# Performance work log

Hardware: AMD Instinct MI355X
Metric: run time of the kernel (lower is better)

The kernel has to match this reference:

```python
import jax, jax.numpy as jnp
import numpy as np

N = 100000      # nodes
E = 1600000     # directed edges (avg degree 16)
DIN, DH, DOUT = 128, 128, 64


def gcn_conv(x, W, b, src, dst, n):
    """PyG GCNConv: out = D^{-1/2} (A + I) D^{-1/2} (x @ W) + b.
    src/dst already include self-loops."""
    deg = jax.ops.segment_sum(jnp.ones_like(src, dtype=x.dtype), dst, num_segments=n)
    dinv = jnp.where(deg > 0, jax.lax.rsqrt(deg), jnp.zeros_like(deg))
    norm = dinv[src] * dinv[dst]                      # [E+N]
    h = x @ W                                         # [N, dout] linear first (PyG)
    msg = h[src] * norm[:, None]                      # gather + scale, [E+N, dout]
    return jax.ops.segment_sum(msg, dst, num_segments=n) + b


def setup_inputs() -> dict:
    key = jax.random.key(0)
    k1, k2, k3 = jax.random.split(key, 3)
    x = jax.random.normal(k1, (N, DIN), dtype=jnp.float32)
    edge_index = jax.random.randint(k2, (2, E), 0, N, dtype=jnp.int64)
    kw1, kw2 = jax.random.split(k3)
    # glorot-style init for the two GCN linear weights
    W1 = jax.random.normal(kw1, (DIN, DH), dtype=jnp.float32) * (1.0 / np.sqrt(DIN))
    b1 = jnp.zeros((DH,), dtype=jnp.float32)
    W2 = jax.random.normal(kw2, (DH, DOUT), dtype=jnp.float32) * (1.0 / np.sqrt(DH))
    b2 = jnp.zeros((DOUT,), dtype=jnp.float32)
    return {"x": x, "W1": W1, "b1": b1, "W2": W2, "b2": b2, "edge_index": edge_index}


def reference(x, W1, b1, W2, b2, edge_index):
    n = x.shape[0]
    loops = jnp.arange(n, dtype=edge_index.dtype)
    src = jnp.concatenate([edge_index[0], loops])     # add self-loops
    dst = jnp.concatenate([edge_index[1], loops])
    h = jax.nn.relu(gcn_conv(x, W1, b1, src, dst, n))
    return gcn_conv(h, W2, b2, src, dst, n)
```

## Files before the change

kernel.cpp:

```cpp
#include <hip/hip_runtime.h>

#define N_NODES 100000
#define N_EDGES 1600000
#define BUCKET_SHIFT 9
#define NB 196
#define BIN_BLOCKS 782
#define GEMM_BLOCKS 1563
#define BCAP 10240

typedef short bf16x8 __attribute__((ext_vector_type(8)));
typedef float f32x4 __attribute__((ext_vector_type(4)));

__device__ __forceinline__ unsigned short f2bf(float f) {
    unsigned int u = __float_as_uint(f);
    unsigned int r = (u + 0x7FFFu + ((u >> 16) & 1u)) >> 16;
    return (unsigned short)r;
}
__device__ __forceinline__ float bf2f(unsigned short b) {
    return __uint_as_float(((unsigned int)b) << 16);
}

__global__ __launch_bounds__(256) void k_tw(const float* __restrict__ W1, const float* __restrict__ W2,
                                            unsigned short* __restrict__ w1t, unsigned short* __restrict__ w2t,
                                            int* __restrict__ bcur) {
    int t = blockIdx.x * 256 + threadIdx.x;
    if (t < 16384) {
        int k = t >> 7, c = t & 127;
        w1t[c * 128 + k] = f2bf(W1[t]);
    } else if (t < 24576) {
        int i = t - 16384;
        int k = i >> 6, c = i & 63;
        w2t[c * 128 + k] = f2bf(W2[i]);
    } else if (t - 24576 < NB) {
        bcur[t - 24576] = 0;
    }
}

__global__ __launch_bounds__(256) void k_bin(const int* __restrict__ src, const int* __restrict__ dst,
                                             int* __restrict__ bcur, int* __restrict__ ebuf) {
    __shared__ int hist[NB];
    __shared__ int lbase[NB];
    int t = threadIdx.x;
    int e0 = blockIdx.x * 2048 + t;
    int s[8], d[8];
#pragma unroll
    for (int j = 0; j < 8; ++j) {
        int e = e0 + j * 256;
        bool ok = e < N_EDGES;
        s[j] = ok ? src[e] : -1;
        d[j] = ok ? dst[e] : 0;
    }
    if (t < NB) hist[t] = 0;
    __syncthreads();
#pragma unroll
    for (int j = 0; j < 8; ++j)
        if (s[j] >= 0) atomicAdd(&hist[d[j] >> BUCKET_SHIFT], 1);
    __syncthreads();
    if (t < NB && hist[t] > 0) lbase[t] = atomicAdd(&bcur[t], hist[t]);
    __syncthreads();
    if (t < NB) hist[t] = 0;
    __syncthreads();
#pragma unroll
    for (int j = 0; j < 8; ++j) {
        if (s[j] >= 0) {
            int b = d[j] >> BUCKET_SHIFT;
            int r = lbase[b] + atomicAdd(&hist[b], 1);
            if (r < BCAP) ebuf[b * BCAP + r] = ((d[j] & 511) << 17) | s[j];
        }
    }
}

__global__ __launch_bounds__(256) void k_bfill3(const int* __restrict__ ebuf, const int* __restrict__ bcur,
                                                int* __restrict__ rowptr, float* __restrict__ dinv,
                                                int* __restrict__ csr) {
    __shared__ int sc[256];
    __shared__ int cnt[512];
    __shared__ int cur[512];
    int b = blockIdx.x, t = threadIdx.x;
    int node0 = b << BUCKET_SHIFT;
    int v = (t < NB) ? bcur[t] : 0;
    sc[t] = v;
    cnt[t] = 0;
    cnt[t + 256] = 0;
    __syncthreads();
    for (int off = 1; off < 256; off <<= 1) {
        int u = (t >= off) ? sc[t - off] : 0;
        __syncthreads();
        sc[t] += u;
        __syncthreads();
    }
    int cb = bcur[b];
    int s0 = sc[b] - cb;
    int ctot = cb > BCAP ? BCAP : cb;
    const int* eb = ebuf + b * BCAP;
    for (int i = t; i < ctot; i += 256) atomicAdd(&cnt[eb[i] >> 17], 1);
    __syncthreads();
    int c0 = cnt[2 * t], c1 = cnt[2 * t + 1];
    int ps = c0 + c1;
    sc[t] = ps;
    __syncthreads();
    for (int off = 1; off < 256; off <<= 1) {
        int u = (t >= off) ? sc[t - off] : 0;
        __syncthreads();
        sc[t] += u;
        __syncthreads();
    }
    int e0x = sc[t] - ps;
    int p0 = s0 + e0x, p1 = s0 + e0x + c0;
    int n0 = node0 + 2 * t, n1 = n0 + 1;
    if (n0 < N_NODES) { rowptr[n0] = p0; dinv[n0] = rsqrtf(1.0f + (float)c0); }
    if (n1 < N_NODES) { rowptr[n1] = p1; dinv[n1] = rsqrtf(1.0f + (float)c1); }
    if (b == NB - 1 && t == 0) rowptr[N_NODES] = N_EDGES;
    cur[2 * t] = p0;
    cur[2 * t + 1] = p1;
    __syncthreads();
    for (int i = t; i < ctot; i += 256) {
        int e = eb[i];
        int p = atomicAdd(&cur[e >> 17], 1);
        csr[p] = e & 0x1FFFF;
    }
}

__global__ __launch_bounds__(256) void k_gemm1(const float* __restrict__ x, const unsigned short* __restrict__ w1t,
                                               const float* __restrict__ dinv, unsigned short* __restrict__ hsb) {
    __shared__ unsigned short Xl[64 * 136];
    __shared__ unsigned short Wl[128 * 136];
    int t = threadIdx.x;
    int row0 = blockIdx.x * 64;
    for (int i = t; i < 64 * 32; i += 256) {
        int r = i >> 5, c4 = i & 31;
        int row = row0 + r;
        float4 v = (row < N_NODES) ? ((const float4*)x)[(long long)row * 32 + c4]
                                   : make_float4(0.f, 0.f, 0.f, 0.f);
        ushort4 o;
        o.x = f2bf(v.x); o.y = f2bf(v.y); o.z = f2bf(v.z); o.w = f2bf(v.w);
        *(ushort4*)&Xl[r * 136 + c4 * 4] = o;
    }
    for (int i = t; i < 128 * 16; i += 256) {
        int r = i >> 4, c8 = i & 15;
        *(bf16x8*)&Wl[r * 136 + c8 * 8] = *(const bf16x8*)&w1t[r * 128 + c8 * 8];
    }
    __syncthreads();
    int w = t >> 6, lane = t & 63;
    int nn = lane & 15, quad = lane >> 4;
    bf16x8 a[4];
#pragma unroll
    for (int kt = 0; kt < 4; ++kt)
        a[kt] = *(const bf16x8*)&Xl[(w * 16 + nn) * 136 + kt * 32 + quad * 8];
    f32x4 acc[8];
#pragma unroll
    for (int ct = 0; ct < 8; ++ct) {
        acc[ct] = (f32x4){0.f, 0.f, 0.f, 0.f};
#pragma unroll
        for (int kt = 0; kt < 4; ++kt) {
            bf16x8 b = *(const bf16x8*)&Wl[(ct * 16 + nn) * 136 + kt * 32 + quad * 8];
            acc[ct] = __builtin_amdgcn_mfma_f32_16x16x32_bf16(a[kt], b, acc[ct], 0, 0, 0);
        }
    }
#pragma unroll
    for (int r = 0; r < 4; ++r) {
        int row = row0 + w * 16 + quad * 4 + r;
        float dv = (row < N_NODES) ? dinv[row] : 0.f;
#pragma unroll
        for (int ct = 0; ct < 8; ++ct)
            Xl[(w * 16 + quad * 4 + r) * 136 + ct * 16 + nn] = f2bf(acc[ct][r] * dv);
    }
#pragma unroll
    for (int j = 0; j < 8; ++j) {
        int c = lane + j * 64;
        int r = c >> 5, c4 = c & 31;
        int row = row0 + w * 16 + r;
        if (row < N_NODES)
            ((ushort4*)(hsb + (long long)row * 128))[c4] = *(const ushort4*)&Xl[(w * 16 + r) * 136 + c4 * 4];
    }
}

__global__ __launch_bounds__(256) void k_agg1(const unsigned short* __restrict__ hsb, const int* __restrict__ rowptr,
                                              const int* __restrict__ csr, const float* __restrict__ dinv,
                                              const float* __restrict__ b1, unsigned short* __restrict__ h) {
    int n = (blockIdx.x * 256 + threadIdx.x) >> 6;
    int lane = threadIdx.x & 63;
    if (n >= N_NODES) return;
    int half = lane >> 5, li = lane & 31;
    float a0, a1, a2, a3;
    {
        ushort4 sv = ((const ushort4*)(hsb + (long long)n * 128))[li];
        float z = half ? 0.f : 1.f;
        a0 = z * bf2f(sv.x); a1 = z * bf2f(sv.y); a2 = z * bf2f(sv.z); a3 = z * bf2f(sv.w);
    }
    int k = rowptr[n], end = rowptr[n + 1];
    for (; k + 3 < end; k += 4) {
        int ia = csr[k + half];
        int ib = csr[k + 2 + half];
        ushort4 va = ((const ushort4*)(hsb + (long long)ia * 128))[li];
        ushort4 vb = ((const ushort4*)(hsb + (long long)ib * 128))[li];
        a0 += bf2f(va.x) + bf2f(vb.x);
        a1 += bf2f(va.y) + bf2f(vb.y);
        a2 += bf2f(va.z) + bf2f(vb.z);
        a3 += bf2f(va.w) + bf2f(vb.w);
    }
    for (; k < end; k += 2) {
        int kk = k + half;
        if (kk < end) {
            int idx = csr[kk];
            ushort4 v = ((const ushort4*)(hsb + (long long)idx * 128))[li];
            a0 += bf2f(v.x); a1 += bf2f(v.y); a2 += bf2f(v.z); a3 += bf2f(v.w);
        }
    }
    a0 += __shfl_xor(a0, 32);
    a1 += __shfl_xor(a1, 32);
    a2 += __shfl_xor(a2, 32);
    a3 += __shfl_xor(a3, 32);
    if (half == 0) {
        float dv = dinv[n];
        float4 bb = ((const float4*)b1)[li];
        ushort4 o;
        o.x = f2bf(fmaxf(fmaf(dv, a0, bb.x), 0.f));
        o.y = f2bf(fmaxf(fmaf(dv, a1, bb.y), 0.f));
        o.z = f2bf(fmaxf(fmaf(dv, a2, bb.z), 0.f));
        o.w = f2bf(fmaxf(fmaf(dv, a3, bb.w), 0.f));
        ((ushort4*)(h + (long long)n * 128))[li] = o;
    }
}

__global__ __launch_bounds__(256) void k_gemm2(const unsigned short* __restrict__ h, const unsigned short* __restrict__ w2t,
                                               const float* __restrict__ dinv, unsigned short* __restrict__ gsb) {
    __shared__ unsigned short Hl[64 * 136];
    __shared__ unsigned short Wl[64 * 136];
    int t = threadIdx.x;
    int row0 = blockIdx.x * 64;
    for (int i = t; i < 64 * 16; i += 256) {
        int r = i >> 4, c8 = i & 15;
        int row = row0 + r;
        bf16x8 v = (row < N_NODES) ? *(const bf16x8*)&h[(long long)row * 128 + c8 * 8]
                                   : (bf16x8){0, 0, 0, 0, 0, 0, 0, 0};
        *(bf16x8*)&Hl[r * 136 + c8 * 8] = v;
        *(bf16x8*)&Wl[r * 136 + c8 * 8] = *(const bf16x8*)&w2t[r * 128 + c8 * 8];
    }
    __syncthreads();
    int w = t >> 6, lane = t & 63;
    int nn = lane & 15, quad = lane >> 4;
    bf16x8 a[4];
#pragma unroll
    for (int kt = 0; kt < 4; ++kt)
        a[kt] = *(const bf16x8*)&Hl[(w * 16 + nn) * 136 + kt * 32 + quad * 8];
    f32x4 acc[4];
#pragma unroll
    for (int ct = 0; ct < 4; ++ct) {
        acc[ct] = (f32x4){0.f, 0.f, 0.f, 0.f};
#pragma unroll
        for (int kt = 0; kt < 4; ++kt) {
            bf16x8 b = *(const bf16x8*)&Wl[(ct * 16 + nn) * 136 + kt * 32 + quad * 8];
            acc[ct] = __builtin_amdgcn_mfma_f32_16x16x32_bf16(a[kt], b, acc[ct], 0, 0, 0);
        }
    }
#pragma unroll
    for (int r = 0; r < 4; ++r) {
        int row = row0 + w * 16 + quad * 4 + r;
        float dv = (row < N_NODES) ? dinv[row] : 0.f;
#pragma unroll
        for (int ct = 0; ct < 4; ++ct)
            Hl[(w * 16 + quad * 4 + r) * 136 + ct * 16 + nn] = f2bf(acc[ct][r] * dv);
    }
#pragma unroll
    for (int j = 0; j < 4; ++j) {
        int c = lane + j * 64;
        int r = c >> 4, c4 = c & 15;
        int row = row0 + w * 16 + r;
        if (row < N_NODES)
            ((ushort4*)(gsb + (long long)row * 64))[c4] = *(const ushort4*)&Hl[(w * 16 + r) * 136 + c4 * 4];
    }
}

__global__ __launch_bounds__(256) void k_agg2(const unsigned short* __restrict__ gsb, const int* __restrict__ rowptr,
                                              const int* __restrict__ csr, const float* __restrict__ dinv,
                                              const float* __restrict__ b2, float* __restrict__ out) {
    int n = (blockIdx.x * 256 + threadIdx.x) >> 6;
    int lane = threadIdx.x & 63;
    if (n >= N_NODES) return;
    int q = lane >> 4, li = lane & 15;
    float a0, a1, a2, a3;
    {
        ushort4 sv = ((const ushort4*)(gsb + (long long)n * 64))[li];
        float z = (q == 0) ? 1.f : 0.f;
        a0 = z * bf2f(sv.x); a1 = z * bf2f(sv.y); a2 = z * bf2f(sv.z); a3 = z * bf2f(sv.w);
    }
    int k = rowptr[n], end = rowptr[n + 1];
    for (; k + 7 < end; k += 8) {
        int ia = csr[k + q];
        int ib = csr[k + 4 + q];
        ushort4 va = ((const ushort4*)(gsb + (long long)ia * 64))[li];
        ushort4 vb = ((const ushort4*)(gsb + (long long)ib * 64))[li];
        a0 += bf2f(va.x) + bf2f(vb.x);
        a1 += bf2f(va.y) + bf2f(vb.y);
        a2 += bf2f(va.z) + bf2f(vb.z);
        a3 += bf2f(va.w) + bf2f(vb.w);
    }
    for (; k < end; k += 4) {
        int kk = k + q;
        if (kk < end) {
            int idx = csr[kk];
            ushort4 v = ((const ushort4*)(gsb + (long long)idx * 64))[li];
            a0 += bf2f(v.x); a1 += bf2f(v.y); a2 += bf2f(v.z); a3 += bf2f(v.w);
        }
    }
    a0 += __shfl_xor(a0, 16); a0 += __shfl_xor(a0, 32);
    a1 += __shfl_xor(a1, 16); a1 += __shfl_xor(a1, 32);
    a2 += __shfl_xor(a2, 16); a2 += __shfl_xor(a2, 32);
    a3 += __shfl_xor(a3, 16); a3 += __shfl_xor(a3, 32);
    if (lane < 16) {
        float dv = dinv[n];
        float4 bb = ((const float4*)b2)[li];
        float4 o = make_float4(fmaf(dv, a0, bb.x), fmaf(dv, a1, bb.y),
                               fmaf(dv, a2, bb.z), fmaf(dv, a3, bb.w));
        ((float4*)(out + (long long)n * 64))[li] = o;
    }
}

extern "C" void kernel_launch(void* const* d_in, const int* in_sizes, int n_in,
                              void* d_out, int out_size, void* d_ws, size_t ws_size,
                              hipStream_t stream) {
    const float* x  = (const float*)d_in[0];
    const float* W1 = (const float*)d_in[1];
    const float* b1 = (const float*)d_in[2];
    const float* W2 = (const float*)d_in[3];
    const float* b2 = (const float*)d_in[4];
    const int*   ei = (const int*)d_in[5];
    const int* src = ei;
    const int* dst = ei + N_EDGES;
    float* out = (float*)d_out;

    char* ws = (char*)d_ws;
    int*   csr    = (int*)(ws + 0);
    int*   rowptr = (int*)(ws + 6800000);
    float* dinv   = (float*)(ws + 7200256);
    int*   bcur   = (int*)(ws + 7604352);
    unsigned short* w1t = (unsigned short*)(ws + 7608448);
    unsigned short* w2t = (unsigned short*)(ws + 7641216);
    int*   ebuf   = (int*)(ws + 8388608);
    unsigned short* hsb = (unsigned short*)(ws + 8388608);
    unsigned short* h   = (unsigned short*)(ws + 59588608);
    unsigned short* gsb = hsb;

    k_tw<<<97, 256, 0, stream>>>(W1, W2, w1t, w2t, bcur);
    k_bin<<<BIN_BLOCKS, 256, 0, stream>>>(src, dst, bcur, ebuf);
    k_bfill3<<<NB, 256, 0, stream>>>(ebuf, bcur, rowptr, dinv, csr);

    k_gemm1<<<GEMM_BLOCKS, 256, 0, stream>>>(x, w1t, dinv, hsb);
    k_agg1<<<(N_NODES * 64) / 256, 256, 0, stream>>>(hsb, rowptr, csr, dinv, b1, h);
    k_gemm2<<<GEMM_BLOCKS, 256, 0, stream>>>(h, w2t, dinv, gsb);
    k_agg2<<<(N_NODES * 64) / 256, 256, 0, stream>>>(gsb, rowptr, csr, dinv, b2, out);
}
```

Before: 314.8 us.

## Remap aggregation kernels to sub-wave node groups with 16-byte gathers

Both SpMM aggregation kernels now assign one node to a 16-lane (agg1) or 8-lane (agg2) group instead of a full 64-lane wave. Each lane loads 8 bf16 values with one 16-byte access, and the edge loop is unrolled eight-wide so several independent row gathers are in flight per lane. Because each lane handles all of its node's edges, the cross-lane shuffle reduction is no longer needed. The intent is to cut wasted lanes, reduction overhead and load count, at the cost of more registers per lane and more load imbalance inside a wave when nodes have different degrees.

```diff
diff --git a/kernel.cpp b/kernel.cpp
--- a/kernel.cpp
+++ b/kernel.cpp
@@ -7,9 +7,12 @@
 #define BIN_BLOCKS 782
 #define GEMM_BLOCKS 1563
 #define BCAP 10240
+#define AGG1_BLOCKS 6250
+#define AGG2_BLOCKS 3125
 
 typedef short bf16x8 __attribute__((ext_vector_type(8)));
 typedef float f32x4 __attribute__((ext_vector_type(4)));
+typedef float f32x8 __attribute__((ext_vector_type(8)));
 
 __device__ __forceinline__ unsigned short f2bf(float f) {
     unsigned int u = __float_as_uint(f);
@@ -18,6 +21,16 @@
 }
 __device__ __forceinline__ float bf2f(unsigned short b) {
     return __uint_as_float(((unsigned int)b) << 16);
+}
+__device__ __forceinline__ void acc8(float* a, uint4 v) {
+    a[0] += __uint_as_float(v.x << 16);
+    a[1] += __uint_as_float(v.x & 0xFFFF0000u);
+    a[2] += __uint_as_float(v.y << 16);
+    a[3] += __uint_as_float(v.y & 0xFFFF0000u);
+    a[4] += __uint_as_float(v.z << 16);
+    a[5] += __uint_as_float(v.z & 0xFFFF0000u);
+    a[6] += __uint_as_float(v.w << 16);
+    a[7] += __uint_as_float(v.w & 0xFFFF0000u);
 }
 
 __global__ __launch_bounds__(256) void k_tw(const float* __restrict__ W1, const float* __restrict__ W2,
@@ -178,49 +191,57 @@
 __global__ __launch_bounds__(256) void k_agg1(const unsigned short* __restrict__ hsb, const int* __restrict__ rowptr,
                                               const int* __restrict__ csr, const float* __restrict__ dinv,
                                               const float* __restrict__ b1, unsigned short* __restrict__ h) {
-    int n = (blockIdx.x * 256 + threadIdx.x) >> 6;
-    int lane = threadIdx.x & 63;
-    if (n >= N_NODES) return;
-    int half = lane >> 5, li = lane & 31;
-    float a0, a1, a2, a3;
+    unsigned g = (blockIdx.x * 256 + threadIdx.x) >> 4;
+    unsigned li = threadIdx.x & 15;
+    if (g >= N_NODES) return;
+    unsigned co = li * 8;
+    float a[8];
     {
-        ushort4 sv = ((const ushort4*)(hsb + (long long)n * 128))[li];
-        float z = half ? 0.f : 1.f;
-        a0 = z * bf2f(sv.x); a1 = z * bf2f(sv.y); a2 = z * bf2f(sv.z); a3 = z * bf2f(sv.w);
-    }
-    int k = rowptr[n], end = rowptr[n + 1];
-    for (; k + 3 < end; k += 4) {
-        int ia = csr[k + half];
-        int ib = csr[k + 2 + half];
-        ushort4 va = ((const ushort4*)(hsb + (long long)ia * 128))[li];
-        ushort4 vb = ((const ushort4*)(hsb + (long long)ib * 128))[li];
-        a0 += bf2f(va.x) + bf2f(vb.x);
-        a1 += bf2f(va.y) + bf2f(vb.y);
-        a2 += bf2f(va.z) + bf2f(vb.z);
-        a3 += bf2f(va.w) + bf2f(vb.w);
-    }
-    for (; k < end; k += 2) {
-        int kk = k + half;
-        if (kk < end) {
-            int idx = csr[kk];
-            ushort4 v = ((const ushort4*)(hsb + (long long)idx * 128))[li];
-            a0 += bf2f(v.x); a1 += bf2f(v.y); a2 += bf2f(v.z); a3 += bf2f(v.w);
-        }
-    }
-    a0 += __shfl_xor(a0, 32);
-    a1 += __shfl_xor(a1, 32);
-    a2 += __shfl_xor(a2, 32);
-    a3 += __shfl_xor(a3, 32);
-    if (half == 0) {
-        float dv = dinv[n];
-        float4 bb = ((const float4*)b1)[li];
-        ushort4 o;
-        o.x = f2bf(fmaxf(fmaf(dv, a0, bb.x), 0.f));
-        o.y = f2bf(fmaxf(fmaf(dv, a1, bb.y), 0.f));
-        o.z = f2bf(fmaxf(fmaf(dv, a2, bb.z), 0.f));
-        o.w = f2bf(fmaxf(fmaf(dv, a3, bb.w), 0.f));
-        ((ushort4*)(h + (long long)n * 128))[li] = o;
-    }
+        uint4 sv = *(const uint4*)(hsb + (g << 7) + co);
+        a[0] = __uint_as_float(sv.x << 16);
+        a[1] = __uint_as_float(sv.x & 0xFFFF0000u);
+        a[2] = __uint_as_float(sv.y << 16);
+        a[3] = __uint_as_float(sv.y & 0xFFFF0000u);
+        a[4] = __uint_as_float(sv.z << 16);
+        a[5] = __uint_as_float(sv.z & 0xFFFF0000u);
+        a[6] = __uint_as_float(sv.w << 16);
+        a[7] = __uint_as_float(sv.w & 0xFFFF0000u);
+    }
+    int k = rowptr[g], end = rowptr[g + 1];
+    for (; k + 7 < end; k += 8) {
+        int i0 = csr[k + 0], i1 = csr[k + 1], i2 = csr[k + 2], i3 = csr[k + 3];
+        int i4 = csr[k + 4], i5 = csr[k + 5], i6 = csr[k + 6], i7 = csr[k + 7];
+        uint4 v0 = *(const uint4*)(hsb + (((unsigned)i0) << 7) + co);
+        uint4 v1 = *(const uint4*)(hsb + (((unsigned)i1) << 7) + co);
+        uint4 v2 = *(const uint4*)(hsb + (((unsigned)i2) << 7) + co);
+        uint4 v3 = *(const uint4*)(hsb + (((unsigned)i3) << 7) + co);
+        uint4 v4 = *(const uint4*)(hsb + (((unsigned)i4) << 7) + co);
+        uint4 v5 = *(const uint4*)(hsb + (((unsigned)i5) << 7) + co);
+        uint4 v6 = *(const uint4*)(hsb + (((unsigned)i6) << 7) + co);
+        uint4 v7 = *(const uint4*)(hsb + (((unsigned)i7) << 7) + co);
+        acc8(a, v0); acc8(a, v1); acc8(a, v2); acc8(a, v3);
+        acc8(a, v4); acc8(a, v5); acc8(a, v6); acc8(a, v7);
+    }
+    if (k + 3 < end) {
+        int i0 = csr[k + 0], i1 = csr[k + 1], i2 = csr[k + 2], i3 = csr[k + 3];
+        uint4 v0 = *(const uint4*)(hsb + (((unsigned)i0) << 7) + co);
+        uint4 v1 = *(const uint4*)(hsb + (((unsigned)i1) << 7) + co);
+        uint4 v2 = *(const uint4*)(hsb + (((unsigned)i2) << 7) + co);
+        uint4 v3 = *(const uint4*)(hsb + (((unsigned)i3) << 7) + co);
+        acc8(a, v0); acc8(a, v1); acc8(a, v2); acc8(a, v3);
+        k += 4;
+    }
+    for (; k < end; ++k) {
+        uint4 v = *(const uint4*)(hsb + (((unsigned)csr[k]) << 7) + co);
+        acc8(a, v);
+    }
+    float dv = dinv[g];
+    f32x8 bb = *(const f32x8*)(b1 + li * 8);
+    bf16x8 o;
+#pragma unroll
+    for (int j = 0; j < 8; ++j)
+        o[j] = (short)f2bf(fmaxf(fmaf(dv, a[j], bb[j]), 0.f));
+    *(bf16x8*)(h + (g << 7) + co) = o;
 }
 
 __global__ __launch_bounds__(256) void k_gemm2(const unsigned short* __restrict__ h, const unsigned short* __restrict__ w2t,
@@ -275,46 +296,59 @@
 __global__ __launch_bounds__(256) void k_agg2(const unsigned short* __restrict__ gsb, const int* __restrict__ rowptr,
                                               const int* __restrict__ csr, const float* __restrict__ dinv,
                                               const float* __restrict__ b2, float* __restrict__ out) {
-    int n = (blockIdx.x * 256 + threadIdx.x) >> 6;
-    int lane = threadIdx.x & 63;
-    if (n >= N_NODES) return;
-    int q = lane >> 4, li = lane & 15;
-    float a0, a1, a2, a3;
+    unsigned g = (blockIdx.x * 256 + threadIdx.x) >> 3;
+    unsigned li = threadIdx.x & 7;
+    if (g >= N_NODES) return;
+    unsigned co = li * 8;
+    float a[8];
     {
-        ushort4 sv = ((const ushort4*)(gsb + (long long)n * 64))[li];
-        float z = (q == 0) ? 1.f : 0.f;
-        a0 = z * bf2f(sv.x); a1 = z * bf2f(sv.y); a2 = z * bf2f(sv.z); a3 = z * bf2f(sv.w);
-    }
-    int k = rowptr[n], end = rowptr[n + 1];
+        uint4 sv = *(const uint4*)(gsb + (g << 6) + co);
+        a[0] = __uint_as_float(sv.x << 16);
+        a[1] = __uint_as_float(sv.x & 0xFFFF0000u);
+        a[2] = __uint_as_float(sv.y << 16);
+        a[3] = __uint_as_float(sv.y & 0xFFFF0000u);
+        a[4] = __uint_as_float(sv.z << 16);
+        a[5] = __uint_as_float(sv.z & 0xFFFF0000u);
+        a[6] = __uint_as_float(sv.w << 16);
+        a[7] = __uint_as_float(sv.w & 0xFFFF0000u);
+    }
+    int k = rowptr[g], end = rowptr[g + 1];
     for (; k + 7 < end; k += 8) {
-        int ia = csr[k + q];
-        int ib = csr[k + 4 + q];
-        ushort4 va = ((const ushort4*)(gsb + (long long)ia * 64))[li];
-        ushort4 vb = ((const ushort4*)(gsb + (long long)ib * 64))[li];
-        a0 += bf2f(va.x) + bf2f(vb.x);
-        a1 += bf2f(va.y) + bf2f(vb.y);
-        a2 += bf2f(va.z) + bf2f(vb.z);
-        a3 += bf2f(va.w) + bf2f(vb.w);
-    }
-    for (; k < end; k += 4) {
-        int kk = k + q;
-        if (kk < end) {
-            int idx = csr[kk];
-            ushort4 v = ((const ushort4*)(gsb + (long long)idx * 64))[li];
-            a0 += bf2f(v.x); a1 += bf2f(v.y); a2 += bf2f(v.z); a3 += bf2f(v.w);
-        }
-    }
-    a0 += __shfl_xor(a0, 16); a0 += __shfl_xor(a0, 32);
-    a1 += __shfl_xor(a1, 16); a1 += __shfl_xor(a1, 32);
-    a2 += __shfl_xor(a2, 16); a2 += __shfl_xor(a2, 32);
-    a3 += __shfl_xor(a3, 16); a3 += __shfl_xor(a3, 32);
-    if (lane < 16) {
-        float dv = dinv[n];
-        float4 bb = ((const float4*)b2)[li];
-        float4 o = make_float4(fmaf(dv, a0, bb.x), fmaf(dv, a1, bb.y),
-                               fmaf(dv, a2, bb.z), fmaf(dv, a3, bb.w));
-        ((float4*)(out + (long long)n * 64))[li] = o;
-    }
+        int i0 = csr[k + 0], i1 = csr[k + 1], i2 = csr[k + 2], i3 = csr[k + 3];
+        int i4 = csr[k + 4], i5 = csr[k + 5], i6 = csr[k + 6], i7 = csr[k + 7];
+        uint4 v0 = *(const uint4*)(gsb + (((unsigned)i0) << 6) + co);
+        uint4 v1 = *(const uint4*)(gsb + (((unsigned)i1) << 6) + co);
+        uint4 v2 = *(const uint4*)(gsb + (((unsigned)i2) << 6) + co);
+        uint4 v3 = *(const uint4*)(gsb + (((unsigned)i3) << 6) + co);
+        uint4 v4 = *(const uint4*)(gsb + (((unsigned)i4) << 6) + co);
+        uint4 v5 = *(const uint4*)(gsb + (((unsigned)i5) << 6) + co);
+        uint4 v6 = *(const uint4*)(gsb + (((unsigned)i6) << 6) + co);
+        uint4 v7 = *(const uint4*)(gsb + (((unsigned)i7) << 6) + co);
+        acc8(a, v0); acc8(a, v1); acc8(a, v2); acc8(a, v3);
+        acc8(a, v4); acc8(a, v5); acc8(a, v6); acc8(a, v7);
+    }
+    if (k + 3 < end) {
+        int i0 = csr[k + 0], i1 = csr[k + 1], i2 = csr[k + 2], i3 = csr[k + 3];
+        uint4 v0 = *(const uint4*)(gsb + (((unsigned)i0) << 6) + co);
+        uint4 v1 = *(const uint4*)(gsb + (((unsigned)i1) << 6) + co);
+        uint4 v2 = *(const uint4*)(gsb + (((unsigned)i2) << 6) + co);
+        uint4 v3 = *(const uint4*)(gsb + (((unsigned)i3) << 6) + co);
+        acc8(a, v0); acc8(a, v1); acc8(a, v2); acc8(a, v3);
+        k += 4;
+    }
+    for (; k < end; ++k) {
+        uint4 v = *(const uint4*)(gsb + (((unsigned)csr[k]) << 6) + co);
+        acc8(a, v);
+    }
+    float dv = dinv[g];
+    f32x8 bb = *(const f32x8*)(b2 + li * 8);
+    float4 o0 = make_float4(fmaf(dv, a[0], bb[0]), fmaf(dv, a[1], bb[1]),
+                            fmaf(dv, a[2], bb[2]), fmaf(dv, a[3], bb[3]));
+    float4 o1 = make_float4(fmaf(dv, a[4], bb[4]), fmaf(dv, a[5], bb[5]),
+                            fmaf(dv, a[6], bb[6]), fmaf(dv, a[7], bb[7]));
+    float* op = out + ((long long)g << 6) + co;
+    *(float4*)op = o0;
+    *(float4*)(op + 4) = o1;
 }
 
 extern "C" void kernel_launch(void* const* d_in, const int* in_sizes, int n_in,
@@ -347,7 +381,7 @@
     k_bfill3<<<NB, 256, 0, stream>>>(ebuf, bcur, rowptr, dinv, csr);
 
     k_gemm1<<<GEMM_BLOCKS, 256, 0, stream>>>(x, w1t, dinv, hsb);
-    k_agg1<<<(N_NODES * 64) / 256, 256, 0, stream>>>(hsb, rowptr, csr, dinv, b1, h);
+    k_agg1<<<AGG1_BLOCKS, 256, 0, stream>>>(hsb, rowptr, csr, dinv, b1, h);
     k_gemm2<<<GEMM_BLOCKS, 256, 0, stream>>>(h, w2t, dinv, gsb);
-    k_agg2<<<(N_NODES * 64) / 256, 256, 0, stream>>>(gsb, rowptr, csr, dinv, b2, out);
-}
+    k_agg2<<<AGG2_BLOCKS, 256, 0, stream>>>(gsb, rowptr, csr, dinv, b2, out);
+}
```

Result: faster. 269.1 us (-14.5%).
